# Performance work log

Measured on AMD Instinct MI355X. Metric: run time of the kernel, lower is better.

The kernel has to match this reference:

```python
import jax, jax.numpy as jnp
import numpy as np

N_USERS = 100000
N_MOVIES = 100000
N_EDGES = 1000000
HIDDEN = 128


def setup_inputs() -> dict:
    key = jax.random.key(0)
    k1, k2, k3, k4, k5, k6, k7 = jax.random.split(key, 7)
    user_features = jax.random.normal(k1, (N_USERS, HIDDEN), dtype=jnp.float32)
    movie_features = jax.random.normal(k2, (N_MOVIES, HIDDEN), dtype=jnp.float32)
    src = jax.random.randint(k3, (N_EDGES,), 0, N_USERS, dtype=jnp.int64 if jax.config.jax_enable_x64 else jnp.int32)
    dst = jax.random.randint(k4, (N_EDGES,), 0, N_MOVIES, dtype=jnp.int64 if jax.config.jax_enable_x64 else jnp.int32)
    edge_index = jnp.stack([src, dst], axis=0)
    # Linear(2*HIDDEN, HIDDEN) params, torch-style init (kaiming uniform ~ U(-1/sqrt(fan_in), 1/sqrt(fan_in)))
    b1_bound = 1.0 / np.sqrt(2 * HIDDEN)
    W1 = jax.random.uniform(k5, (2 * HIDDEN, HIDDEN), minval=-b1_bound, maxval=b1_bound, dtype=jnp.float32)
    b1 = jax.random.uniform(k6, (HIDDEN,), minval=-b1_bound, maxval=b1_bound, dtype=jnp.float32)
    b2_bound = 1.0 / np.sqrt(HIDDEN)
    k8, k9 = jax.random.split(k7)
    W2 = jax.random.uniform(k8, (HIDDEN, 1), minval=-b2_bound, maxval=b2_bound, dtype=jnp.float32)
    b2 = jax.random.uniform(k9, (1,), minval=-b2_bound, maxval=b2_bound, dtype=jnp.float32)
    return {"user_features": user_features, "movie_features": movie_features,
            "edge_index": edge_index, "W1": W1, "b1": b1, "W2": W2, "b2": b2}


def reference(user_features, movie_features, edge_index, W1, b1, W2, b2):
    # Gather endpoint features per edge: [E, H] each
    u = user_features[edge_index[0]]
    m = movie_features[edge_index[1]]
    edge_feats = jnp.concatenate([u, m], axis=1)  # [E, 2H]
    h = jax.nn.relu(edge_feats @ W1 + b1)         # [E, H]
    out = h @ W2 + b2                             # [E, 1]
    return out.reshape(-1)
```

## Files before the change

kernel.cpp:

```cpp
#include <hip/hip_runtime.h>
#include <hip/hip_bf16.h>

typedef short s8v __attribute__((ext_vector_type(8)));
typedef float f4v __attribute__((ext_vector_type(4)));

__device__ __forceinline__ unsigned int bfround(float f) {
    unsigned int x = __float_as_uint(f);
    return (x + 0x7fffu + ((x >> 16) & 1u)) >> 16;
}

__device__ __forceinline__ float i8f(unsigned int w, int k) {
    return (float)((int)(signed char)(w >> (8 * k)));
}

__global__ __launch_bounds__(256) void proj_kernel(
    const float* __restrict__ userf, const float* __restrict__ movief,
    const float* __restrict__ W1, const float* __restrict__ b1,
    uint2* __restrict__ Pu, uint2* __restrict__ Pm,
    float* __restrict__ SU, float* __restrict__ SM, int ntiles)
{
    const int half = blockIdx.x & 1;
    const float* __restrict__ feat = half ? movief : userf;
    uint2* __restrict__ P = half ? Pm : Pu;
    float* __restrict__ S = half ? SM : SU;
    const int whalf = half << 7;

    const int lane = threadIdx.x & 63;
    const int m    = lane & 15;
    const int q    = lane >> 4;

    s8v  bfrag[8][4];
    float bias_v[8];
    #pragma unroll
    for (int t = 0; t < 8; ++t) {
        int col = t * 16 + m;
        bias_v[t] = half ? b1[col] : 0.0f;
        #pragma unroll
        for (int c = 0; c < 4; ++c) {
            s8v bf;
            #pragma unroll
            for (int j = 0; j < 8; ++j)
                bf[j] = (short)bfround(W1[(size_t)(whalf + c * 32 + q * 8 + j) * 128 + col]);
            bfrag[t][c] = bf;
        }
    }

    const int widh = (blockIdx.x >> 1) * 4 + (threadIdx.x >> 6);
    const int nwh  = (gridDim.x >> 1) * 4;

    for (int tile = widh; tile < ntiles; tile += nwh) {
        const float4* arow = (const float4*)feat + (size_t)tile * 512;

        float4 a[4][2];
        #pragma unroll
        for (int c = 0; c < 4; ++c) {
            a[c][0] = arow[m * 32 + c * 8 + q * 2 + 0];
            a[c][1] = arow[m * 32 + c * 8 + q * 2 + 1];
        }

        f4v acc[8];
        #pragma unroll
        for (int t = 0; t < 8; ++t)
            acc[t] = (f4v){bias_v[t], bias_v[t], bias_v[t], bias_v[t]};

        #pragma unroll
        for (int c = 0; c < 4; ++c) {
            s8v af;
            af[0] = (short)bfround(a[c][0].x); af[1] = (short)bfround(a[c][0].y);
            af[2] = (short)bfround(a[c][0].z); af[3] = (short)bfround(a[c][0].w);
            af[4] = (short)bfround(a[c][1].x); af[5] = (short)bfround(a[c][1].y);
            af[6] = (short)bfround(a[c][1].z); af[7] = (short)bfround(a[c][1].w);
            #pragma unroll
            for (int t = 0; t < 8; ++t)
                acc[t] = __builtin_amdgcn_mfma_f32_16x16x32_bf16(af, bfrag[t][c], acc[t], 0, 0, 0);
        }

        #pragma unroll
        for (int r = 0; r < 4; ++r) {
            float mx = 0.0f;
            #pragma unroll
            for (int t = 0; t < 8; ++t) mx = fmaxf(mx, fabsf(acc[t][r]));
            #pragma unroll
            for (int off = 1; off < 16; off <<= 1)
                mx = fmaxf(mx, __shfl_xor(mx, off, 64));
            float inv = mx > 0.0f ? 127.0f / mx : 0.0f;

            unsigned int lo = 0, hi = 0;
            #pragma unroll
            for (int t = 0; t < 4; ++t) {
                lo |= ((unsigned int)(__float2int_rn(acc[t][r]     * inv) & 0xff)) << (8 * t);
                hi |= ((unsigned int)(__float2int_rn(acc[t + 4][r] * inv) & 0xff)) << (8 * t);
            }
            int row = tile * 16 + q * 4 + r;
            P[(size_t)row * 16 + m] = make_uint2(lo, hi);
            if (m == 0) S[row] = mx * (1.0f / 127.0f);
        }
    }
}

__global__ __launch_bounds__(256) void edge_kernel(
    const int* __restrict__ src, const int* __restrict__ dst,
    const uint2* __restrict__ Pu, const uint2* __restrict__ Pm,
    const float* __restrict__ SU, const float* __restrict__ SM,
    const float* __restrict__ W2, const float* __restrict__ b2,
    float* __restrict__ out)
{
    const int lane = threadIdx.x & 63;
    const int L    = lane & 15;
    const int g    = lane >> 4;
    const int eg   = (blockIdx.x * 4 + (threadIdx.x >> 6)) * 16 + g * 4;

    float w2v[8];
    #pragma unroll
    for (int j = 0; j < 8; ++j) w2v[j] = W2[j * 16 + L];

    int si[4], di[4];
    #pragma unroll
    for (int i = 0; i < 4; ++i) { si[i] = src[eg + i]; di[i] = dst[eg + i]; }

    uint2 pu[4], pm[4];
    float scu[4], scm[4];
    #pragma unroll
    for (int i = 0; i < 4; ++i) {
        pu[i] = Pu[(size_t)si[i] * 16 + L];
        pm[i] = Pm[(size_t)di[i] * 16 + L];
        scu[i] = SU[si[i]];
        scm[i] = SM[di[i]];
    }

    float res[4];
    #pragma unroll
    for (int i = 0; i < 4; ++i) {
        const unsigned int uw[2] = {pu[i].x, pu[i].y};
        const unsigned int mw[2] = {pm[i].x, pm[i].y};
        float acc = 0.0f;
        #pragma unroll
        for (int v = 0; v < 2; ++v) {
            #pragma unroll
            for (int k = 0; k < 4; ++k) {
                float h = fmaf(scu[i], i8f(uw[v], k), scm[i] * i8f(mw[v], k));
                acc = fmaf(fmaxf(h, 0.0f), w2v[v * 4 + k], acc);
            }
        }
        #pragma unroll
        for (int off = 1; off < 16; off <<= 1)
            acc += __shfl_xor(acc, off, 64);
        res[i] = acc;
    }

    if (L == 0) {
        float bb = b2[0];
        *(float4*)(out + eg) = make_float4(res[0] + bb, res[1] + bb, res[2] + bb, res[3] + bb);
    }
}

extern "C" void kernel_launch(void* const* d_in, const int* in_sizes, int n_in,
                              void* d_out, int out_size, void* d_ws, size_t ws_size,
                              hipStream_t stream) {
    const float* userf  = (const float*)d_in[0];
    const float* movief = (const float*)d_in[1];
    const int*   eidx   = (const int*)d_in[2];
    const float* W1     = (const float*)d_in[3];
    const float* b1     = (const float*)d_in[4];
    const float* W2     = (const float*)d_in[5];
    const float* b2     = (const float*)d_in[6];
    float* out = (float*)d_out;

    const int NU = in_sizes[0] / 128;
    const int NM = in_sizes[1] / 128;
    const int E  = in_sizes[2] / 2;

    uint2* Pu = (uint2*)d_ws;
    uint2* Pm = Pu + (size_t)NU * 16;
    float* SU = (float*)(Pm + (size_t)NM * 16);
    float* SM = SU + NU;

    proj_kernel<<<512, 256, 0, stream>>>(userf, movief, W1, b1, Pu, Pm, SU, SM, NU / 16);
    edge_kernel<<<E / 64, 256, 0, stream>>>(eidx, eidx + E, Pu, Pm, SU, SM, W2, b2, out);
}
```

Baseline: 200.8 us.

## Prepack W1 bf16 fragments once and launch one wave per projection tile

Adds a small pre-kernel that converts W1 to bf16 and lays it out in the MFMA B-fragment order once. The projection kernel then streams these fragments per k-chunk instead of keeping all 32 fragments resident in registers, and drops the persistent grid-stride loop in favour of one wave per 16-row tile with launch bounds allowing 3 blocks per CU. The aim is to cut register pressure and raise occupancy so the feature loads are better hidden, at the cost of reloading the weights from cache in every wave and an extra kernel launch.

New measurement: 192.9 us. -3.9%, faster.

```diff
diff --git a/kernel.cpp b/kernel.cpp
--- a/kernel.cpp
+++ b/kernel.cpp
@@ -13,88 +13,101 @@
     return (float)((int)(signed char)(w >> (8 * k)));
 }
 
-__global__ __launch_bounds__(256) void proj_kernel(
+__global__ __launch_bounds__(256) void pack_w(const float* __restrict__ W1,
+                                              uint4* __restrict__ WF)
+{
+    const int half = blockIdx.x;
+    #pragma unroll
+    for (int iter = 0; iter < 8; ++iter) {
+        int idx  = iter * 256 + threadIdx.x;
+        int lane = idx & 63;
+        int t    = (idx >> 6) & 7;
+        int c    = idx >> 9;
+        int q = lane >> 4, m = lane & 15;
+        unsigned int w[4];
+        #pragma unroll
+        for (int jj = 0; jj < 4; ++jj) {
+            float lo = W1[(size_t)(half * 128 + c * 32 + q * 8 + 2 * jj    ) * 128 + t * 16 + m];
+            float hi = W1[(size_t)(half * 128 + c * 32 + q * 8 + 2 * jj + 1) * 128 + t * 16 + m];
+            w[jj] = bfround(lo) | (bfround(hi) << 16);
+        }
+        WF[(size_t)half * 2048 + idx] = make_uint4(w[0], w[1], w[2], w[3]);
+    }
+}
+
+__global__ __launch_bounds__(256, 3) void proj_kernel(
     const float* __restrict__ userf, const float* __restrict__ movief,
-    const float* __restrict__ W1, const float* __restrict__ b1,
+    const uint4* __restrict__ WF, const float* __restrict__ b1,
     uint2* __restrict__ Pu, uint2* __restrict__ Pm,
     float* __restrict__ SU, float* __restrict__ SM, int ntiles)
 {
     const int half = blockIdx.x & 1;
+    const int tile = (blockIdx.x >> 1) * 4 + (threadIdx.x >> 6);
+    if (tile >= ntiles) return;
     const float* __restrict__ feat = half ? movief : userf;
     uint2* __restrict__ P = half ? Pm : Pu;
     float* __restrict__ S = half ? SM : SU;
-    const int whalf = half << 7;
 
     const int lane = threadIdx.x & 63;
     const int m    = lane & 15;
     const int q    = lane >> 4;
 
-    s8v  bfrag[8][4];
+    const float4* arow = (const float4*)feat + (size_t)tile * 512;
+    float4 a[4][2];
+    #pragma unroll
+    for (int c = 0; c < 4; ++c) {
+        a[c][0] = arow[m * 32 + c * 8 + q * 2 + 0];
+        a[c][1] = arow[m * 32 + c * 8 + q * 2 + 1];
+    }
+
     float bias_v[8];
     #pragma unroll
-    for (int t = 0; t < 8; ++t) {
-        int col = t * 16 + m;
-        bias_v[t] = half ? b1[col] : 0.0f;
+    for (int t = 0; t < 8; ++t)
+        bias_v[t] = half ? b1[t * 16 + m] : 0.0f;
+
+    f4v acc[8];
+    #pragma unroll
+    for (int t = 0; t < 8; ++t)
+        acc[t] = (f4v){bias_v[t], bias_v[t], bias_v[t], bias_v[t]};
+
+    const uint4* wf = WF + (size_t)half * 2048;
+    #pragma unroll
+    for (int c = 0; c < 4; ++c) {
+        uint4 fr[8];
         #pragma unroll
-        for (int c = 0; c < 4; ++c) {
-            s8v bf;
-            #pragma unroll
-            for (int j = 0; j < 8; ++j)
-                bf[j] = (short)bfround(W1[(size_t)(whalf + c * 32 + q * 8 + j) * 128 + col]);
-            bfrag[t][c] = bf;
-        }
+        for (int t = 0; t < 8; ++t)
+            fr[t] = wf[(c * 8 + t) * 64 + lane];
+
+        s8v af;
+        af[0] = (short)bfround(a[c][0].x); af[1] = (short)bfround(a[c][0].y);
+        af[2] = (short)bfround(a[c][0].z); af[3] = (short)bfround(a[c][0].w);
+        af[4] = (short)bfround(a[c][1].x); af[5] = (short)bfround(a[c][1].y);
+        af[6] = (short)bfround(a[c][1].z); af[7] = (short)bfround(a[c][1].w);
+
+        #pragma unroll
+        for (int t = 0; t < 8; ++t)
+            acc[t] = __builtin_amdgcn_mfma_f32_16x16x32_bf16(af, *(const s8v*)&fr[t], acc[t], 0, 0, 0);
     }
 
-    const int widh = (blockIdx.x >> 1) * 4 + (threadIdx.x >> 6);
-    const int nwh  = (gridDim.x >> 1) * 4;
+    #pragma unroll
+    for (int r = 0; r < 4; ++r) {
+        float mx = 0.0f;
+        #pragma unroll
+        for (int t = 0; t < 8; ++t) mx = fmaxf(mx, fabsf(acc[t][r]));
+        #pragma unroll
+        for (int off = 1; off < 16; off <<= 1)
+            mx = fmaxf(mx, __shfl_xor(mx, off, 64));
+        float inv = mx > 0.0f ? 127.0f / mx : 0.0f;
 
-    for (int tile = widh; tile < ntiles; tile += nwh) {
-        const float4* arow = (const float4*)feat + (size_t)tile * 512;
-
-        float4 a[4][2];
+        unsigned int lo = 0, hi = 0;
         #pragma unroll
-        for (int c = 0; c < 4; ++c) {
-            a[c][0] = arow[m * 32 + c * 8 + q * 2 + 0];
-            a[c][1] = arow[m * 32 + c * 8 + q * 2 + 1];
+        for (int t = 0; t < 4; ++t) {
+            lo |= ((unsigned int)(__float2int_rn(acc[t][r]     * inv) & 0xff)) << (8 * t);
+            hi |= ((unsigned int)(__float2int_rn(acc[t + 4][r] * inv) & 0xff)) << (8 * t);
         }
-
-        f4v acc[8];
-        #pragma unroll
-        for (int t = 0; t < 8; ++t)
-            acc[t] = (f4v){bias_v[t], bias_v[t], bias_v[t], bias_v[t]};
-
-        #pragma unroll
-        for (int c = 0; c < 4; ++c) {
-            s8v af;
-            af[0] = (short)bfround(a[c][0].x); af[1] = (short)bfround(a[c][0].y);
-            af[2] = (short)bfround(a[c][0].z); af[3] = (short)bfround(a[c][0].w);
-            af[4] = (short)bfround(a[c][1].x); af[5] = (short)bfround(a[c][1].y);
-            af[6] = (short)bfround(a[c][1].z); af[7] = (short)bfround(a[c][1].w);
-            #pragma unroll
-            for (int t = 0; t < 8; ++t)
-                acc[t] = __builtin_amdgcn_mfma_f32_16x16x32_bf16(af, bfrag[t][c], acc[t], 0, 0, 0);
-        }
-
-        #pragma unroll
-        for (int r = 0; r < 4; ++r) {
-            float mx = 0.0f;
-            #pragma unroll
-            for (int t = 0; t < 8; ++t) mx = fmaxf(mx, fabsf(acc[t][r]));
-            #pragma unroll
-            for (int off = 1; off < 16; off <<= 1)
-                mx = fmaxf(mx, __shfl_xor(mx, off, 64));
-            float inv = mx > 0.0f ? 127.0f / mx : 0.0f;
-
-            unsigned int lo = 0, hi = 0;
-            #pragma unroll
-            for (int t = 0; t < 4; ++t) {
-                lo |= ((unsigned int)(__float2int_rn(acc[t][r]     * inv) & 0xff)) << (8 * t);
-                hi |= ((unsigned int)(__float2int_rn(acc[t + 4][r] * inv) & 0xff)) << (8 * t);
-            }
-            int row = tile * 16 + q * 4 + r;
-            P[(size_t)row * 16 + m] = make_uint2(lo, hi);
-            if (m == 0) S[row] = mx * (1.0f / 127.0f);
-        }
+        int row = tile * 16 + q * 4 + r;
+        P[(size_t)row * 16 + m] = make_uint2(lo, hi);
+        if (m == 0) S[row] = mx * (1.0f / 127.0f);
     }
 }
 
@@ -174,7 +187,12 @@
     uint2* Pm = Pu + (size_t)NU * 16;
     float* SU = (float*)(Pm + (size_t)NM * 16);
     float* SM = SU + NU;
+    uint4* WF = (uint4*)(SM + NM);
 
-    proj_kernel<<<512, 256, 0, stream>>>(userf, movief, W1, b1, Pu, Pm, SU, SM, NU / 16);
+    const int ntiles = NU / 16;
+    const int nblk   = 2 * ((ntiles + 3) / 4);
+
+    pack_w<<<2, 256, 0, stream>>>(W1, WF);
+    proj_kernel<<<nblk, 256, 0, stream>>>(userf, movief, WF, b1, Pu, Pm, SU, SM, ntiles);
     edge_kernel<<<E / 64, 256, 0, stream>>>(eidx, eidx + E, Pu, Pm, SU, SM, W2, b2, out);
 }
```
